# Kernel optimization log

Hardware: AMD Instinct MI355X
Metric: run time of the kernel (lower is better)

## Reference

```python
import jax, jax.numpy as jnp
import numpy as np

HIDDEN = 1024
NUM_HEADS = 16
HEAD_DIM = HIDDEN // NUM_HEADS


def rotary_cos_sin(seq_len, head_dim, dtype=jnp.float32):
    inv_freq = 1.0 / (10000.0 ** (jnp.arange(0, head_dim, 2, dtype=dtype) / head_dim))
    t = jnp.arange(seq_len, dtype=dtype)
    freqs = jnp.einsum('i,j->ij', t, inv_freq)          # [S, hd/2]
    emb = jnp.concatenate([freqs, freqs], axis=-1)      # [S, hd]
    return jnp.cos(emb), jnp.sin(emb)


def apply_rotary(x, cos, sin):
    # x: [B, H, S, hd]; cos/sin: [S, hd]
    x1, x2 = jnp.split(x, 2, axis=-1)
    x_rot = jnp.concatenate([-x2, x1], axis=-1)
    return x * cos + x_rot * sin


def setup_inputs() -> dict:
    key = jax.random.key(0)
    ks = jax.random.split(key, 5)
    S, B = 2048, 2
    x = jax.random.normal(ks[0], (S, B, HIDDEN), dtype=jnp.float32)
    s = 1.0 / np.sqrt(HIDDEN)
    W_qkv = jax.random.uniform(ks[1], (HIDDEN, 3 * HIDDEN), jnp.float32, -s, s)
    b_qkv = jax.random.uniform(ks[2], (3 * HIDDEN,), jnp.float32, -s, s)
    W_out = jax.random.uniform(ks[3], (HIDDEN, HIDDEN), jnp.float32, -s, s)
    b_out = jax.random.uniform(ks[4], (HIDDEN,), jnp.float32, -s, s)
    return {"x": x, "W_qkv": W_qkv, "b_qkv": b_qkv, "W_out": W_out, "b_out": b_out}


def reference(x, W_qkv, b_qkv, W_out, b_out):
    S, B, D = x.shape
    scale = HEAD_DIM ** -0.5
    qkv = x @ W_qkv + b_qkv                               # [S, B, 3D]
    qkv = qkv.reshape(S, B, NUM_HEADS, 3 * HEAD_DIM)
    q, k, v = jnp.split(qkv, 3, axis=-1)                  # each [S, B, H, hd]
    q = q.transpose(1, 2, 0, 3)                           # [B, H, S, hd]
    k = k.transpose(1, 2, 0, 3)
    v = v.transpose(1, 2, 0, 3)
    cos, sin = rotary_cos_sin(S, HEAD_DIM, x.dtype)
    q = apply_rotary(q, cos, sin)
    k = apply_rotary(k, cos, sin)
    scores = jnp.einsum('bhqd,bhkd->bhqk', q, k) * scale  # [B, H, S, S]
    weights = jax.nn.softmax(scores, axis=-1)
    attn = jnp.einsum('bhqk,bhkd->bhqd', weights, v)      # [B, H, S, hd]
    attn = attn.transpose(2, 0, 1, 3).reshape(S, B, D)    # [S, B, D]
    return attn @ W_out + b_out
```

## Files before the change

kernel.cpp:

```cpp
#include <hip/hip_runtime.h>

typedef unsigned short u16;
typedef __attribute__((ext_vector_type(8))) short bf16x8;
typedef __attribute__((ext_vector_type(4))) float f32x4;
typedef __attribute__((ext_vector_type(16))) float f32x16;

#define S_LEN 2048
#define BATCH 2
#define HID 1024
#define NH 16
#define HD 64
#define MROWS 4096
#define QKV_N 3072
#define QSCALE 0.18033688011112042f

__device__ __forceinline__ u16 f2bf(float f) {
  unsigned u = __float_as_uint(f);
  u += 0x7fffu + ((u >> 16) & 1u);
  return (u16)(u >> 16);
}

__device__ __forceinline__ float bf2f(u16 u) {
  return __uint_as_float((unsigned)u << 16);
}

__device__ __forceinline__ float fexp2(float x) {
  float r; asm("v_exp_f32 %0, %1" : "=v"(r) : "v"(x)); return r;
}

__device__ __forceinline__ unsigned cvtpk(float lo, float hi) {
  unsigned r; asm("v_cvt_pk_bf16_f32 %0, %1, %2" : "=v"(r) : "v"(lo), "v"(hi)); return r;
}

__device__ __forceinline__ void gl2lds16(const u16* src, u16* lds) {
  __builtin_amdgcn_global_load_lds((__attribute__((address_space(1))) void*)(void*)src,
                                   (__attribute__((address_space(3))) void*)(void*)lds,
                                   16, 0, 0);
}

__device__ __forceinline__ void castT_body(const float* __restrict__ W, u16* __restrict__ Wt,
                                           int Ncols, int Krows, int bx, int by,
                                           float (*tile)[33]) {
  int c0 = bx * 32, r0 = by * 32;
  int tx = threadIdx.x & 31, ty = threadIdx.x >> 5;
  #pragma unroll
  for (int i = 0; i < 4; ++i)
    tile[ty + i * 8][tx] = W[(size_t)(r0 + ty + i * 8) * Ncols + c0 + tx];
  __syncthreads();
  #pragma unroll
  for (int i = 0; i < 4; ++i) {
    int a = ty + i * 8;
    Wt[(size_t)(c0 + a) * Krows + r0 + tx] = f2bf(tile[tx][a]);
  }
}

__global__ __launch_bounds__(256) void prep(
    const float* __restrict__ x, const float* __restrict__ W_qkv,
    const float* __restrict__ W_out, u16* __restrict__ xb,
    u16* __restrict__ Wqt, u16* __restrict__ Wot, float2* __restrict__ rope) {
  __shared__ float tile[32][33];
  const int bid = blockIdx.x;
  if (bid < 2048) {
    int i = bid * 256 + threadIdx.x;
    const float4* p = (const float4*)x;
    float4 a = p[2 * i], b = p[2 * i + 1];
    union { u16 us[8]; uint4 v; } o;
    o.us[0] = f2bf(a.x); o.us[1] = f2bf(a.y); o.us[2] = f2bf(a.z); o.us[3] = f2bf(a.w);
    o.us[4] = f2bf(b.x); o.us[5] = f2bf(b.y); o.us[6] = f2bf(b.z); o.us[7] = f2bf(b.w);
    *(uint4*)&xb[8 * i] = o.v;
  } else if (bid < 2048 + 3072) {
    int r = bid - 2048;
    castT_body(W_qkv, Wqt, QKV_N, HID, r % 96, r / 96, tile);
  } else if (bid < 2048 + 3072 + 1024) {
    int r = bid - (2048 + 3072);
    castT_body(W_out, Wot, HID, HID, r % 32, r / 32, tile);
  } else {
    int i = (bid - 6144) * 256 + threadIdx.x;
    int s = i >> 5, j = i & 31;
    float invf = fexp2(-(float)(2 * j) * (13.287712379549449f / 64.0f));
    float ang = (float)s * invf;
    rope[i] = make_float2(cosf(ang), sinf(ang));
  }
}

__global__ __launch_bounds__(256, 2) void gemm_qkv(
    const u16* __restrict__ A, const u16* __restrict__ Bt,
    const float* __restrict__ bias, const float2* __restrict__ rope,
    u16* __restrict__ Qb, u16* __restrict__ Kb, u16* __restrict__ Vb) {
  __shared__ u16 As[128 * 32];
  __shared__ u16 Bs[128 * 32];
  const int tid = threadIdx.x;
  const int lane = tid & 63, wid = tid >> 6;
  const int g = lane >> 4, l15 = lane & 15;
  const int bm0 = blockIdx.x * 128, bn0 = blockIdx.y * 128;
  const int wm = wid >> 1, wn = wid & 1;

  f32x4 acc[4][4] = {};
  for (int kt = 0; kt < 32; ++kt) {
    const int k0 = kt * 32;
    __syncthreads();
    #pragma unroll
    for (int it = 0; it < 2; ++it) {
      int s = it * 256 + tid;
      gl2lds16(A  + (size_t)(bm0 + (s >> 2)) * 1024 + k0 + (s & 3) * 8, &As[s * 8]);
      gl2lds16(Bt + (size_t)(bn0 + (s >> 2)) * 1024 + k0 + (s & 3) * 8, &Bs[s * 8]);
    }
    __syncthreads();
    bf16x8 af[4], bfr[4];
    #pragma unroll
    for (int m = 0; m < 4; ++m) af[m]  = *(const bf16x8*)&As[(wm * 64 + m * 16 + l15) * 32 + g * 8];
    #pragma unroll
    for (int n = 0; n < 4; ++n) bfr[n] = *(const bf16x8*)&Bs[(wn * 64 + n * 16 + l15) * 32 + g * 8];
    #pragma unroll
    for (int m = 0; m < 4; ++m)
      #pragma unroll
      for (int n = 0; n < 4; ++n)
        acc[m][n] = __builtin_amdgcn_mfma_f32_16x16x32_bf16(af[m], bfr[n], acc[m][n], 0, 0, 0);
  }

  const int cw0 = bn0 + wn * 64;
  const int gi = cw0 >> 6;
  const int h = gi / 3, tt = gi % 3;
  float bs[4];
  #pragma unroll
  for (int n = 0; n < 4; ++n) bs[n] = bias[cw0 + n * 16 + l15];
  const size_t hb = (size_t)h * (S_LEN * HD);

  if (tt == 2) {
    #pragma unroll
    for (int m = 0; m < 4; ++m)
      #pragma unroll
      for (int reg = 0; reg < 4; ++reg) {
        int r = bm0 + wm * 64 + m * 16 + g * 4 + reg;
        int srow = r >> 1, b = r & 1;
        size_t o = (size_t)(b * NH) * (S_LEN * HD) + hb + (size_t)srow * HD;
        #pragma unroll
        for (int n = 0; n < 4; ++n)
          Vb[o + n * 16 + l15] = f2bf(acc[m][n][reg] + bs[n]);
      }
  } else {
    u16* dst = (tt == 0) ? Qb : Kb;
    const float scl = (tt == 0) ? QSCALE : 1.0f;
    #pragma unroll
    for (int m = 0; m < 4; ++m)
      #pragma unroll
      for (int reg = 0; reg < 4; ++reg) {
        int r = bm0 + wm * 64 + m * 16 + g * 4 + reg;
        int srow = r >> 1, b = r & 1;
        size_t o = (size_t)(b * NH) * (S_LEN * HD) + hb + (size_t)srow * HD;
        #pragma unroll
        for (int n = 0; n < 2; ++n) {
          int dlo = n * 16 + l15;
          float2 cs = rope[srow * 32 + dlo];
          float v1 = acc[m][n][reg] + bs[n];
          float v2 = acc[m][n + 2][reg] + bs[n + 2];
          dst[o + dlo]      = f2bf((v1 * cs.x - v2 * cs.y) * scl);
          dst[o + dlo + 32] = f2bf((v2 * cs.x + v1 * cs.y) * scl);
        }
      }
  }
}

__global__ __launch_bounds__(256) void transpose_v(const u16* __restrict__ Vb, u16* __restrict__ Vt) {
  __shared__ u16 t[64][72];
  const int bh = blockIdx.y, s0 = blockIdx.x * 64;
  const size_t base = (size_t)bh * S_LEN * HD;
  const int tid = threadIdx.x;
  #pragma unroll
  for (int it = 0; it < 2; ++it) {
    int sl = it * 256 + tid;
    int r = sl >> 3, cg = sl & 7;
    union { uint4 v; u16 us[8]; } u;
    u.v = *(const uint4*)&Vb[base + (size_t)(s0 + r) * HD + cg * 8];
    #pragma unroll
    for (int j = 0; j < 8; ++j) t[cg * 8 + j][r] = u.us[j];
  }
  __syncthreads();
  #pragma unroll
  for (int it = 0; it < 2; ++it) {
    int sl = it * 256 + tid;
    int d = sl >> 3, sg = sl & 7;
    union { uint4 v; u16 us[8]; } u;
    #pragma unroll
    for (int j = 0; j < 8; ++j) u.us[j] = t[d][sg * 8 + j];
    *(uint4*)&Vt[(size_t)bh * HD * S_LEN + (size_t)d * S_LEN + s0 + sg * 8] = u.v;
  }
}

__global__ __launch_bounds__(256, 4) void attn_fwd(
    const u16* __restrict__ Qb, const u16* __restrict__ Kb,
    const u16* __restrict__ Vt, u16* __restrict__ part0,
    u16* __restrict__ part1, float2* __restrict__ stats) {
  __shared__ u16 Ks[2][64 * 64];
  __shared__ u16 Vs[2][64 * 64];
  const int tid = threadIdx.x;
  const int lane = tid & 63, wid = tid >> 6;
  const int l31 = lane & 31, h = lane >> 5;
  const int pp = blockIdx.x & 63;
  const int bh = pp >> 1, split = pp & 1;
  const int kt0 = split * 16;
  const int qw0 = (blockIdx.x >> 6) * 128 + wid * 32;
  const u16* Qp = Qb + ((size_t)bh * S_LEN + qw0) * HD;
  const u16* Kp = Kb + (size_t)bh * S_LEN * HD;
  const u16* Vp = Vt + (size_t)bh * HD * S_LEN;

  const int sA = tid, sB = tid + 256;
  const int srA = sA >> 3, srB = sB >> 3;
  const int sswA = (sA & 7) ^ (srA & 7), sswB = (sB & 7) ^ (srB & 7);
  #define SIGMA(sr) (((sr >> 4) & 1) * 16 + ((sr >> 2) & 1) * 8 \
                   + (((sr) & 3) | (((sr >> 3) & 1) << 2)) + ((sr) >> 5) * 32)
  const u16* kgA = Kp + (size_t)SIGMA(srA) * HD + sswA * 8;
  const u16* kgB = Kp + (size_t)SIGMA(srB) * HD + sswB * 8;
  const u16* vgA = Vp + (size_t)srA * S_LEN + sswA * 8;
  const u16* vgB = Vp + (size_t)srB * S_LEN + sswB * 8;
  #undef SIGMA

  bf16x8 qf0 = *(const bf16x8*)&Qp[(size_t)l31 * HD +  0 + h * 8];
  bf16x8 qf1 = *(const bf16x8*)&Qp[(size_t)l31 * HD + 16 + h * 8];
  bf16x8 qf2 = *(const bf16x8*)&Qp[(size_t)l31 * HD + 32 + h * 8];
  bf16x8 qf3 = *(const bf16x8*)&Qp[(size_t)l31 * HD + 48 + h * 8];

  f32x16 po0 = {}, po1 = {};
  float mrun = -INFINITY, lrun = 0.f;

  gl2lds16(kgA + (size_t)kt0 * 64 * HD, &Ks[0][sA * 8]);
  gl2lds16(kgB + (size_t)kt0 * 64 * HD, &Ks[0][sB * 8]);
  gl2lds16(vgA + kt0 * 64, &Vs[0][sA * 8]);
  gl2lds16(vgB + kt0 * 64, &Vs[0][sB * 8]);
  __syncthreads();

  for (int i = 0; i < 16; ++i) {
    const int bb = i & 1;
    if (i + 1 < 16) {
      const size_t ko = (size_t)(kt0 + i + 1) * 64 * HD;
      const int vo = (kt0 + i + 1) * 64;
      gl2lds16(kgA + ko, &Ks[bb ^ 1][sA * 8]);
      gl2lds16(kgB + ko, &Ks[bb ^ 1][sB * 8]);
      gl2lds16(vgA + vo, &Vs[bb ^ 1][sA * 8]);
      gl2lds16(vgB + vo, &Vs[bb ^ 1][sB * 8]);
    }
    const u16* KsB = Ks[bb];
    const u16* VsB = Vs[bb];

    f32x16 s0 = {}, s1 = {};
    __builtin_amdgcn_s_setprio(1);
    #pragma unroll
    for (int s = 0; s < 4; ++s) {
      const bf16x8 qf = (s == 0) ? qf0 : (s == 1) ? qf1 : (s == 2) ? qf2 : qf3;
      const int csw = ((2 * s + h) ^ (l31 & 7)) * 8;
      bf16x8 kf0 = *(const bf16x8*)&KsB[l31 * 64 + csw];
      s0 = __builtin_amdgcn_mfma_f32_32x32x16_bf16(kf0, qf, s0, 0, 0, 0);
      bf16x8 kf1 = *(const bf16x8*)&KsB[(32 + l31) * 64 + csw];
      s1 = __builtin_amdgcn_mfma_f32_32x32x16_bf16(kf1, qf, s1, 0, 0, 0);
    }
    __builtin_amdgcn_s_setprio(0);

    float tm = -INFINITY;
    #pragma unroll
    for (int r = 0; r < 16; ++r) tm = fmaxf(tm, fmaxf(s0[r], s1[r]));
    tm = fmaxf(tm, __shfl_xor(tm, 32));

    if (!__all(tm <= mrun + 8.f)) {
      float mnew = fmaxf(mrun, tm);
      float alpha = fexp2(mrun - mnew);
      mrun = mnew;
      lrun *= alpha;
      #pragma unroll
      for (int r = 0; r < 16; ++r) {
        float ar = __shfl(alpha, (r & 3) + 8 * (r >> 2) + 4 * h);
        po0[r] *= ar;
        po1[r] *= ar;
      }
    }

    float rs = 0.f;
    unsigned pwa[8], pwb[8];
    #pragma unroll
    for (int w = 0; w < 8; ++w) {
      float a = fexp2(s0[2 * w] - mrun), b = fexp2(s0[2 * w + 1] - mrun);
      rs += a + b;
      pwa[w] = cvtpk(a, b);
    }
    #pragma unroll
    for (int w = 0; w < 8; ++w) {
      float a = fexp2(s1[2 * w] - mrun), b = fexp2(s1[2 * w + 1] - mrun);
      rs += a + b;
      pwb[w] = cvtpk(a, b);
    }
    rs += __shfl_xor(rs, 32);
    lrun += rs;

    __builtin_amdgcn_s_setprio(1);
    #pragma unroll
    for (int s = 0; s < 4; ++s) {
      union { unsigned w[4]; bf16x8 v; } pf;
      if (s == 0)      { pf.w[0] = pwa[0]; pf.w[1] = pwa[1]; pf.w[2] = pwa[2]; pf.w[3] = pwa[3]; }
      else if (s == 1) { pf.w[0] = pwa[4]; pf.w[1] = pwa[5]; pf.w[2] = pwa[6]; pf.w[3] = pwa[7]; }
      else if (s == 2) { pf.w[0] = pwb[0]; pf.w[1] = pwb[1]; pf.w[2] = pwb[2]; pf.w[3] = pwb[3]; }
      else             { pf.w[0] = pwb[4]; pf.w[1] = pwb[5]; pf.w[2] = pwb[6]; pf.w[3] = pwb[7]; }
      const int csw = ((2 * s + h) ^ (l31 & 7)) * 8;
      bf16x8 vf0 = *(const bf16x8*)&VsB[l31 * 64 + csw];
      po0 = __builtin_amdgcn_mfma_f32_32x32x16_bf16(pf.v, vf0, po0, 0, 0, 0);
      bf16x8 vf1 = *(const bf16x8*)&VsB[(32 + l31) * 64 + csw];
      po1 = __builtin_amdgcn_mfma_f32_32x32x16_bf16(pf.v, vf1, po1, 0, 0, 0);
    }
    __builtin_amdgcn_s_setprio(0);
    __syncthreads();
  }

  u16* part = split ? part1 : part0;
  if (h == 0)
    stats[(size_t)split * (32 * 2048) + (size_t)bh * 2048 + qw0 + l31] =
        make_float2(mrun, lrun);
  #pragma unroll
  for (int r = 0; r < 16; ++r) {
    int q = qw0 + (r & 3) + 8 * (r >> 2) + 4 * h;
    size_t o = ((size_t)bh * 2048 + q) * 64 + l31;
    part[o]      = f2bf(po0[r]);
    part[o + 32] = f2bf(po1[r]);
  }
}

__global__ void attn_combine(const u16* __restrict__ part0, const u16* __restrict__ part1,
                             const float2* __restrict__ stats, u16* __restrict__ attn2d) {
  int t = blockIdx.x * 256 + threadIdx.x;
  int bh = t >> 14, r = t & 16383, q = r >> 3, dc = r & 7;
  int b = bh >> 4, h = bh & 15;
  float2 s0 = stats[bh * 2048 + q];
  float2 s1 = stats[32 * 2048 + bh * 2048 + q];
  float M = fmaxf(s0.x, s1.x);
  float w0 = fexp2(s0.x - M), w1 = fexp2(s1.x - M);
  float inv = 1.f / (w0 * s0.y + w1 * s1.y);
  w0 *= inv; w1 *= inv;
  size_t off = ((size_t)bh * 2048 + q) * 64 + dc * 8;
  union { uint4 v; u16 us[8]; } a, c, o;
  a.v = *(const uint4*)&part0[off];
  c.v = *(const uint4*)&part1[off];
  #pragma unroll
  for (int j = 0; j < 8; ++j)
    o.us[j] = f2bf(w0 * bf2f(a.us[j]) + w1 * bf2f(c.us[j]));
  *(uint4*)&attn2d[((size_t)q * BATCH + b) * HID + h * HD + dc * 8] = o.v;
}

__global__ __launch_bounds__(256, 2) void gemm_out(
    const u16* __restrict__ A, const u16* __restrict__ Bt,
    const float* __restrict__ bias, float* __restrict__ out) {
  __shared__ u16 As[128 * 32];
  __shared__ u16 Bs[64 * 32];
  const int tid = threadIdx.x;
  const int lane = tid & 63, wid = tid >> 6;
  const int g = lane >> 4, l15 = lane & 15;
  const int bm0 = blockIdx.x * 128, bn0 = blockIdx.y * 64;

  f32x4 acc[2][4] = {};
  for (int kt = 0; kt < 32; ++kt) {
    const int k0 = kt * 32;
    __syncthreads();
    #pragma unroll
    for (int it = 0; it < 2; ++it) {
      int s = it * 256 + tid;
      gl2lds16(A + (size_t)(bm0 + (s >> 2)) * 1024 + k0 + (s & 3) * 8, &As[s * 8]);
    }
    gl2lds16(Bt + (size_t)(bn0 + (tid >> 2)) * 1024 + k0 + (tid & 3) * 8, &Bs[tid * 8]);
    __syncthreads();
    bf16x8 af[2], bfr[4];
    #pragma unroll
    for (int m = 0; m < 2; ++m) af[m]  = *(const bf16x8*)&As[(wid * 32 + m * 16 + l15) * 32 + g * 8];
    #pragma unroll
    for (int n = 0; n < 4; ++n) bfr[n] = *(const bf16x8*)&Bs[(n * 16 + l15) * 32 + g * 8];
    #pragma unroll
    for (int m = 0; m < 2; ++m)
      #pragma unroll
      for (int n = 0; n < 4; ++n)
        acc[m][n] = __builtin_amdgcn_mfma_f32_16x16x32_bf16(af[m], bfr[n], acc[m][n], 0, 0, 0);
  }
  #pragma unroll
  for (int n = 0; n < 4; ++n) {
    int c = bn0 + n * 16 + l15;
    float bv = bias[c];
    #pragma unroll
    for (int m = 0; m < 2; ++m)
      #pragma unroll
      for (int reg = 0; reg < 4; ++reg) {
        int r = bm0 + wid * 32 + m * 16 + g * 4 + reg;
        out[(size_t)r * HID + c] = acc[m][n][reg] + bv;
      }
  }
}

extern "C" void kernel_launch(void* const* d_in, const int* in_sizes, int n_in,
                              void* d_out, int out_size, void* d_ws, size_t ws_size,
                              hipStream_t stream) {
  const float* x     = (const float*)d_in[0];
  const float* W_qkv = (const float*)d_in[1];
  const float* b_qkv = (const float*)d_in[2];
  const float* W_out = (const float*)d_in[3];
  const float* b_out = (const float*)d_in[4];
  float* out = (float*)d_out;

  char* ws = (char*)d_ws;
  size_t off = 0;
  auto carve = [&](size_t bytes) { void* p = ws + off; off += (bytes + 255) & ~(size_t)255; return p; };
  u16* xb      = (u16*)carve((size_t)MROWS * HID * 2);
  u16* Wqt     = (u16*)carve((size_t)QKV_N * HID * 2);
  u16* Wot     = (u16*)carve((size_t)HID * HID * 2);
  float2* rope = (float2*)carve((size_t)S_LEN * 32 * 8);
  u16* Qb      = (u16*)carve((size_t)BATCH * NH * S_LEN * HD * 2);
  u16* Kb      = (u16*)carve((size_t)BATCH * NH * S_LEN * HD * 2);
  u16* Vb      = (u16*)carve((size_t)BATCH * NH * S_LEN * HD * 2);
  u16* Vt      = (u16*)carve((size_t)BATCH * NH * S_LEN * HD * 2);
  u16* attn2d  = (u16*)carve((size_t)MROWS * HID * 2);
  float2* stats= (float2*)carve((size_t)2 * 32 * 2048 * 8);

  prep<<<6400, 256, 0, stream>>>(x, W_qkv, W_out, xb, Wqt, Wot, rope);
  gemm_qkv<<<dim3(MROWS / 128, QKV_N / 128), 256, 0, stream>>>(xb, Wqt, b_qkv, rope, Qb, Kb, Vb);
  transpose_v<<<dim3(S_LEN / 64, BATCH * NH), 256, 0, stream>>>(Vb, Vt);
  attn_fwd<<<1024, 256, 0, stream>>>(Qb, Kb, Vt, xb, Vb, stats);
  attn_combine<<<2048, 256, 0, stream>>>(xb, Vb, stats, attn2d);
  gemm_out<<<dim3(MROWS / 128, HID / 64), 256, 0, stream>>>(attn2d, Wot, b_out, out);
}
```

Before: 128.3 us.

## Fuse V transpose into QKV GEMM epilogue and shrink output GEMM tiles

The QKV GEMM now stages V tiles in a swizzled shared-memory buffer and writes them directly in transposed [B,H,D,S] layout. This removes the separate transpose_v kernel and its extra global round trip. The output GEMM moves from 128x64 to 64x64 tiles with a higher occupancy bound, giving more blocks for better GPU fill at the cost of less operand reuse per block. The added 16KB of shared memory in gemm_qkv may reduce its occupancy.

```diff
diff --git a/kernel.cpp b/kernel.cpp
--- a/kernel.cpp
+++ b/kernel.cpp
@@ -86,9 +86,10 @@
 __global__ __launch_bounds__(256, 2) void gemm_qkv(
     const u16* __restrict__ A, const u16* __restrict__ Bt,
     const float* __restrict__ bias, const float2* __restrict__ rope,
-    u16* __restrict__ Qb, u16* __restrict__ Kb, u16* __restrict__ Vb) {
+    u16* __restrict__ Qb, u16* __restrict__ Kb, u16* __restrict__ VtOut) {
   __shared__ u16 As[128 * 32];
   __shared__ u16 Bs[128 * 32];
+  __shared__ u16 vt[2][64][64];
   const int tid = threadIdx.x;
   const int lane = tid & 63, wid = tid >> 6;
   const int g = lane >> 4, l15 = lane & 15;
@@ -131,12 +132,13 @@
     for (int m = 0; m < 4; ++m)
       #pragma unroll
       for (int reg = 0; reg < 4; ++reg) {
-        int r = bm0 + wm * 64 + m * 16 + g * 4 + reg;
-        int srow = r >> 1, b = r & 1;
-        size_t o = (size_t)(b * NH) * (S_LEN * HD) + hb + (size_t)srow * HD;
+        int rl = wm * 64 + m * 16 + g * 4 + reg;
+        int srow = rl >> 1, b = reg & 1;
         #pragma unroll
-        for (int n = 0; n < 4; ++n)
-          Vb[o + n * 16 + l15] = f2bf(acc[m][n][reg] + bs[n]);
+        for (int n = 0; n < 4; ++n) {
+          int d = n * 16 + l15;
+          vt[b][d][srow ^ ((d & 7) << 3)] = f2bf(acc[m][n][reg] + bs[n]);
+        }
       }
   } else {
     u16* dst = (tt == 0) ? Qb : Kb;
@@ -159,31 +161,17 @@
         }
       }
   }
-}
-
-__global__ __launch_bounds__(256) void transpose_v(const u16* __restrict__ Vb, u16* __restrict__ Vt) {
-  __shared__ u16 t[64][72];
-  const int bh = blockIdx.y, s0 = blockIdx.x * 64;
-  const size_t base = (size_t)bh * S_LEN * HD;
-  const int tid = threadIdx.x;
-  #pragma unroll
-  for (int it = 0; it < 2; ++it) {
-    int sl = it * 256 + tid;
-    int r = sl >> 3, cg = sl & 7;
-    union { uint4 v; u16 us[8]; } u;
-    u.v = *(const uint4*)&Vb[base + (size_t)(s0 + r) * HD + cg * 8];
-    #pragma unroll
-    for (int j = 0; j < 8; ++j) t[cg * 8 + j][r] = u.us[j];
-  }
   __syncthreads();
-  #pragma unroll
-  for (int it = 0; it < 2; ++it) {
-    int sl = it * 256 + tid;
-    int d = sl >> 3, sg = sl & 7;
-    union { uint4 v; u16 us[8]; } u;
-    #pragma unroll
-    for (int j = 0; j < 8; ++j) u.us[j] = t[d][sg * 8 + j];
-    *(uint4*)&Vt[(size_t)bh * HD * S_LEN + (size_t)d * S_LEN + s0 + sg * 8] = u.v;
+  if (tt == 2) {
+    const int vtid = wm * 64 + lane;
+    const int s0g = bm0 >> 1;
+    #pragma unroll
+    for (int it = 0; it < 8; ++it) {
+      int task = vtid + it * 128;
+      int b = task >> 9, d = (task >> 3) & 63, ch = task & 7;
+      uint4 v = *(const uint4*)&vt[b][d][(ch ^ (d & 7)) * 8];
+      *(uint4*)&VtOut[((size_t)(b * NH + h) * HD + d) * S_LEN + s0g + ch * 8] = v;
+    }
   }
 }
 
@@ -342,49 +330,40 @@
   *(uint4*)&attn2d[((size_t)q * BATCH + b) * HID + h * HD + dc * 8] = o.v;
 }
 
-__global__ __launch_bounds__(256, 2) void gemm_out(
+__global__ __launch_bounds__(256, 4) void gemm_out(
     const u16* __restrict__ A, const u16* __restrict__ Bt,
     const float* __restrict__ bias, float* __restrict__ out) {
-  __shared__ u16 As[128 * 32];
+  __shared__ u16 As[64 * 32];
   __shared__ u16 Bs[64 * 32];
   const int tid = threadIdx.x;
   const int lane = tid & 63, wid = tid >> 6;
   const int g = lane >> 4, l15 = lane & 15;
-  const int bm0 = blockIdx.x * 128, bn0 = blockIdx.y * 64;
-
-  f32x4 acc[2][4] = {};
+  const int bm0 = blockIdx.x * 64, bn0 = blockIdx.y * 64;
+
+  f32x4 acc[4] = {};
   for (int kt = 0; kt < 32; ++kt) {
     const int k0 = kt * 32;
     __syncthreads();
-    #pragma unroll
-    for (int it = 0; it < 2; ++it) {
-      int s = it * 256 + tid;
-      gl2lds16(A + (size_t)(bm0 + (s >> 2)) * 1024 + k0 + (s & 3) * 8, &As[s * 8]);
-    }
+    gl2lds16(A  + (size_t)(bm0 + (tid >> 2)) * 1024 + k0 + (tid & 3) * 8, &As[tid * 8]);
     gl2lds16(Bt + (size_t)(bn0 + (tid >> 2)) * 1024 + k0 + (tid & 3) * 8, &Bs[tid * 8]);
     __syncthreads();
-    bf16x8 af[2], bfr[4];
-    #pragma unroll
-    for (int m = 0; m < 2; ++m) af[m]  = *(const bf16x8*)&As[(wid * 32 + m * 16 + l15) * 32 + g * 8];
+    bf16x8 af = *(const bf16x8*)&As[(wid * 16 + l15) * 32 + g * 8];
+    bf16x8 bfr[4];
     #pragma unroll
     for (int n = 0; n < 4; ++n) bfr[n] = *(const bf16x8*)&Bs[(n * 16 + l15) * 32 + g * 8];
     #pragma unroll
-    for (int m = 0; m < 2; ++m)
-      #pragma unroll
-      for (int n = 0; n < 4; ++n)
-        acc[m][n] = __builtin_amdgcn_mfma_f32_16x16x32_bf16(af[m], bfr[n], acc[m][n], 0, 0, 0);
+    for (int n = 0; n < 4; ++n)
+      acc[n] = __builtin_amdgcn_mfma_f32_16x16x32_bf16(af, bfr[n], acc[n], 0, 0, 0);
   }
   #pragma unroll
   for (int n = 0; n < 4; ++n) {
     int c = bn0 + n * 16 + l15;
     float bv = bias[c];
     #pragma unroll
-    for (int m = 0; m < 2; ++m)
-      #pragma unroll
-      for (int reg = 0; reg < 4; ++reg) {
-        int r = bm0 + wid * 32 + m * 16 + g * 4 + reg;
-        out[(size_t)r * HID + c] = acc[m][n][reg] + bv;
-      }
+    for (int reg = 0; reg < 4; ++reg) {
+      int r = bm0 + wid * 16 + g * 4 + reg;
+      out[(size_t)r * HID + c] = acc[n][reg] + bv;
+    }
   }
 }
 
@@ -407,15 +386,14 @@
   float2* rope = (float2*)carve((size_t)S_LEN * 32 * 8);
   u16* Qb      = (u16*)carve((size_t)BATCH * NH * S_LEN * HD * 2);
   u16* Kb      = (u16*)carve((size_t)BATCH * NH * S_LEN * HD * 2);
-  u16* Vb      = (u16*)carve((size_t)BATCH * NH * S_LEN * HD * 2);
+  u16* part1   = (u16*)carve((size_t)BATCH * NH * S_LEN * HD * 2);
   u16* Vt      = (u16*)carve((size_t)BATCH * NH * S_LEN * HD * 2);
   u16* attn2d  = (u16*)carve((size_t)MROWS * HID * 2);
   float2* stats= (float2*)carve((size_t)2 * 32 * 2048 * 8);
 
   prep<<<6400, 256, 0, stream>>>(x, W_qkv, W_out, xb, Wqt, Wot, rope);
-  gemm_qkv<<<dim3(MROWS / 128, QKV_N / 128), 256, 0, stream>>>(xb, Wqt, b_qkv, rope, Qb, Kb, Vb);
-  transpose_v<<<dim3(S_LEN / 64, BATCH * NH), 256, 0, stream>>>(Vb, Vt);
-  attn_fwd<<<1024, 256, 0, stream>>>(Qb, Kb, Vt, xb, Vb, stats);
-  attn_combine<<<2048, 256, 0, stream>>>(xb, Vb, stats, attn2d);
-  gemm_out<<<dim3(MROWS / 128, HID / 64), 256, 0, stream>>>(attn2d, Wot, b_out, out);
-}
+  gemm_qkv<<<dim3(MROWS / 128, QKV_N / 128), 256, 0, stream>>>(xb, Wqt, b_qkv, rope, Qb, Kb, Vt);
+  attn_fwd<<<1024, 256, 0, stream>>>(Qb, Kb, Vt, xb, part1, stats);
+  attn_combine<<<2048, 256, 0, stream>>>(xb, part1, stats, attn2d);
+  gemm_out<<<dim3(MROWS / 64, HID / 64), 256, 0, stream>>>(attn2d, Wot, b_out, out);
+}
```

New measurement: 124.6 us. 2.9% less time.
